# Performance work log

Hardware: AMD Instinct MI355X
Metric: run time of the kernel (lower is better)

## Reference

```python
import jax, jax.numpy as jnp
import numpy as np

B, L, H, NL, NRES = 64, 2048, 64, 10, 3
EPS = 1e-5


def _conv1d(x, w, b, pad):
    # x: [B, C, L], w: [O, I, K] (torch layout)
    y = jax.lax.conv_general_dilated(x, w, window_strides=(1,), padding=[(pad, pad)],
                                     dimension_numbers=("NCH", "OIH", "NCH"))
    return y + b[None, :, None]


def _bn(x, g, b, m, v):
    # eval-mode BatchNorm1d over channel dim of [B, C, L]
    scale = (g * jax.lax.rsqrt(v + EPS))[None, :, None]
    return (x - m[None, :, None]) * scale + b[None, :, None]


def _lstm_layer(x, w_ih, w_hh, b_ih, b_hh):
    # x: [T, B, H]; gate order (torch): i, f, g, o
    gates_x = jnp.einsum("tbh,gh->tbg", x, w_ih) + (b_ih + b_hh)  # [T, B, 4H]

    def step(carry, gx):
        h, c = carry
        gates = gx + h @ w_hh.T
        i, f, g, o = jnp.split(gates, 4, axis=-1)
        c = jax.nn.sigmoid(f) * c + jax.nn.sigmoid(i) * jnp.tanh(g)
        h = jax.nn.sigmoid(o) * jnp.tanh(c)
        return (h, c), h

    nb = x.shape[1]
    init = (jnp.zeros((nb, H), x.dtype), jnp.zeros((nb, H), x.dtype))
    _, hs = jax.lax.scan(step, init, gates_x)
    return hs  # [T, B, H]


def setup_inputs() -> dict:
    key = jax.random.key(0)
    ks = jax.random.split(key, 24)
    r = lambda i, shape, s=0.05: jax.random.normal(ks[i], shape, jnp.float32) * s
    inp = {
        "input": jax.random.normal(ks[0], (B, L, 4), jnp.float32),
        "mc": jax.random.uniform(ks[1], (B,), dtype=jnp.float32),
        "conv1_w": r(2, (32, 4, 1), 0.3), "conv1_b": r(3, (32,)),
        "conv2_w": r(4, (64, 32, 1), 0.2), "conv2_b": r(5, (64,)),
        "res_bn1_g": jnp.ones((NRES, 64), jnp.float32), "res_bn1_b": jnp.zeros((NRES, 64), jnp.float32),
        "res_bn1_m": jnp.zeros((NRES, 64), jnp.float32), "res_bn1_v": jnp.ones((NRES, 64), jnp.float32),
        "res_conv1_w": r(6, (NRES, 64, 64, 11)), "res_conv1_b": r(7, (NRES, 64)),
        "res_bn2_g": jnp.ones((NRES, 64), jnp.float32), "res_bn2_b": jnp.zeros((NRES, 64), jnp.float32),
        "res_bn2_m": jnp.zeros((NRES, 64), jnp.float32), "res_bn2_v": jnp.ones((NRES, 64), jnp.float32),
        "res_conv2_w": r(8, (NRES, 64, 64, 11)), "res_conv2_b": r(9, (NRES, 64)),
        "lstm_w_ih": r(10, (NL, 4 * H, H), 0.1), "lstm_w_hh": r(11, (NL, 4 * H, H), 0.1),
        "lstm_b_ih": r(12, (NL, 4 * H)), "lstm_b_hh": r(13, (NL, 4 * H)),
        "out_w": r(14, (H, 2), 0.1), "out_b": r(15, (2,)),
        "l": L,
    }
    return inp


def reference(input, mc, conv1_w, conv1_b, conv2_w, conv2_b,
              res_bn1_g, res_bn1_b, res_bn1_m, res_bn1_v, res_conv1_w, res_conv1_b,
              res_bn2_g, res_bn2_b, res_bn2_m, res_bn2_v, res_conv2_w, res_conv2_b,
              lstm_w_ih, lstm_w_hh, lstm_b_ih, lstm_b_hh, out_w, out_b, l):
    # mc and l are computed/accepted but never used by the original forward.
    x = jnp.transpose(input, (0, 2, 1))                    # [B, 4, L]
    x = jax.nn.relu(_conv1d(x, conv1_w, conv1_b, 0))       # [B, 32, L]
    x = jax.nn.relu(_conv1d(x, conv2_w, conv2_b, 0))       # [B, 64, L]
    for i in range(NRES):                                  # 3 pre-activation residual units
        h = jax.nn.relu(_bn(x, res_bn1_g[i], res_bn1_b[i], res_bn1_m[i], res_bn1_v[i]))
        h = _conv1d(h, res_conv1_w[i], res_conv1_b[i], 5)
        h = jax.nn.relu(_bn(h, res_bn2_g[i], res_bn2_b[i], res_bn2_m[i], res_bn2_v[i]))
        h = _conv1d(h, res_conv2_w[i], res_conv2_b[i], 5)
        x = x + h
    x = jnp.transpose(x, (2, 0, 1))                        # [L, B, 64] (seq-first, like torch LSTM)
    for layer in range(NL):
        x = _lstm_layer(x, lstm_w_ih[layer], lstm_w_hh[layer], lstm_b_ih[layer], lstm_b_hh[layer])
    logits = x[-1] @ out_w + out_b                         # [B, 2]
    return jax.nn.log_softmax(logits, axis=1)
```

## Files before the change

### kernel.cpp

```cpp
#include <hip/hip_runtime.h>
#include <hip/hip_bf16.h>

#define TL 2048
#define NB 64
#define NH 64
#define NLAY 10
#define NRESU 3
#define RSTEP 64

typedef float f32x4 __attribute__((ext_vector_type(4)));
typedef short bhalf8 __attribute__((ext_vector_type(8)));
typedef short bhalf4 __attribute__((ext_vector_type(4)));

__device__ __forceinline__ unsigned short f2bf(float f) {
    unsigned u = __float_as_uint(f);
    unsigned r = u + 0x7fffu + ((u >> 16) & 1u);
    return (unsigned short)(r >> 16);
}
__device__ __forceinline__ float bf2f(unsigned short h) {
    return __uint_as_float(((unsigned)h) << 16);
}
__device__ __forceinline__ float exp2_pos(float x) {
    float r; asm("v_exp_f32 %0, %1" : "=v"(r) : "v"(x)); return r;
}
__device__ __forceinline__ float exp2_neg(float x) {
    float r; asm("v_exp_f32 %0, -%1" : "=v"(r) : "v"(x)); return r;
}

__global__ __launch_bounds__(256) void k_frontend(
    const float* __restrict__ in,
    const float* __restrict__ c1w, const float* __restrict__ c1b,
    const float* __restrict__ c2w, const float* __restrict__ c2b,
    float* __restrict__ x0)
{
    __shared__ float s_c1w[128];
    __shared__ float s_c1b[32];
    __shared__ float s_c2w[64 * 33];
    __shared__ float s_c2b[64];
    __shared__ float h1[64 * 33];
    __shared__ float ot[64 * 65];
    int tid = threadIdx.x;
    int b = blockIdx.x >> 5;
    int l0 = (blockIdx.x & 31) << 6;
    if (tid < 128) s_c1w[tid] = c1w[tid];
    if (tid < 32) s_c1b[tid] = c1b[tid];
    if (tid < 64) s_c2b[tid] = c2b[tid];
    for (int r = tid; r < 2048; r += 256) s_c2w[(r >> 5) * 33 + (r & 31)] = c2w[r];
    __syncthreads();
    if (tid < 64) {
        const float* ip = in + ((size_t)b * TL + l0 + tid) * 4;
        float x0v = ip[0], x1 = ip[1], x2 = ip[2], x3 = ip[3];
#pragma unroll
        for (int o = 0; o < 32; o++) {
            float a = s_c1w[o * 4 + 0] * x0v + s_c1w[o * 4 + 1] * x1 +
                      s_c1w[o * 4 + 2] * x2 + s_c1w[o * 4 + 3] * x3 + s_c1b[o];
            h1[tid * 33 + o] = fmaxf(a, 0.0f);
        }
    }
    __syncthreads();
    {
        int o = tid & 63, lg = tid >> 6;
#pragma unroll
        for (int j = 0; j < 16; j++) {
            int l = lg * 16 + j;
            float a = s_c2b[o];
#pragma unroll
            for (int i = 0; i < 32; i++) a += h1[l * 33 + i] * s_c2w[o * 33 + i];
            ot[o * 65 + l] = fmaxf(a, 0.0f);
        }
    }
    __syncthreads();
    for (int r = 0; r < 16; r++) {
        int idx = tid + 256 * r;
        int c = idx >> 6, l = idx & 63;
        x0[((size_t)b * 64 + c) * TL + l0 + l] = ot[c * 65 + l];
    }
}

__global__ __launch_bounds__(256) void k_prepw_mfma(
    const float* __restrict__ w, unsigned short* __restrict__ wbh, unsigned short* __restrict__ wbl)
{
    int idx = blockIdx.x * 256 + threadIdx.x;
    if (idx >= NRESU * 11 * 64 * 64) return;
    int i = idx & 63;
    int rest = idx >> 6;
    int o = rest & 63;
    rest >>= 6;
    int k = rest % 11;
    int u = rest / 11;
    float v = w[(((size_t)u * 64 + o) * 64 + i) * 11 + k];
    unsigned short hb = f2bf(v);
    float lo = v - bf2f(hb);
    wbh[idx] = hb;
    wbl[idx] = f2bf(lo);
}

#define XTS 76
__global__ __launch_bounds__(256) void k_resconv_mfma(
    const float* __restrict__ in, float* __restrict__ out,
    const unsigned short* __restrict__ wbh, const unsigned short* __restrict__ wbl,
    const float* __restrict__ bias,
    const float* __restrict__ bg, const float* __restrict__ bb,
    const float* __restrict__ bm, const float* __restrict__ bv,
    int accumulate)
{
    __shared__ float sscale[64], sshift[64];
    __shared__ __align__(16) char smem[43776];
    unsigned short* XTH = (unsigned short*)smem;
    unsigned short* XTL = XTH + 144 * XTS;
    float* Yb = (float*)smem;

    int tid = threadIdx.x;
    int b = blockIdx.x >> 4;
    int l0 = (blockIdx.x & 15) << 7;
    int lane = tid & 63;
    int wv = tid >> 6;
    int l15 = lane & 15, l4 = lane >> 4;

    if (tid < 64) {
        float sc = bg[tid] * rsqrtf(bv[tid] + 1e-5f);
        sscale[tid] = sc;
        sshift[tid] = bb[tid] - bm[tid] * sc;
    }
    __syncthreads();

    {
        int lcol = tid & 63;
        int ib = tid >> 6;
#pragma unroll
        for (int it = 0; it < 16; it++) {
            int i = ib + it * 4;
            float sc = sscale[i], sh = sshift[i];
            const float* ip = in + ((size_t)b * 64 + i) * TL;
#pragma unroll
            for (int jc = 0; jc < 3; jc++) {
                int ll = jc * 64 + lcol;
                if (ll < 138) {
                    int l = l0 - 5 + ll;
                    float v = 0.0f;
                    if (l >= 0 && l < TL) v = fmaxf(ip[l] * sc + sh, 0.0f);
                    unsigned short hb = f2bf(v);
                    float lo = v - bf2f(hb);
                    XTH[ll * XTS + i] = hb;
                    XTL[ll * XTS + i] = f2bf(lo);
                }
            }
        }
    }
    __syncthreads();

    f32x4 acc[2][4];
#pragma unroll
    for (int s = 0; s < 2; s++)
#pragma unroll
        for (int ot = 0; ot < 4; ot++) acc[s][ot] = (f32x4){0, 0, 0, 0};

    for (int k = 0; k < 11; k++) {
#pragma unroll
        for (int ic = 0; ic < 2; ic++) {
            bhalf8 ah[2], al[2];
#pragma unroll
            for (int s = 0; s < 2; s++) {
                int row = (wv * 2 + s) * 16 + l15 + k;
                int off = row * XTS + ic * 32 + l4 * 8;
                bhalf4 h0 = *(const bhalf4*)&XTH[off];
                bhalf4 h1v = *(const bhalf4*)&XTH[off + 4];
                bhalf4 lo0 = *(const bhalf4*)&XTL[off];
                bhalf4 lo1 = *(const bhalf4*)&XTL[off + 4];
                ah[s] = (bhalf8){h0[0], h0[1], h0[2], h0[3], h1v[0], h1v[1], h1v[2], h1v[3]};
                al[s] = (bhalf8){lo0[0], lo0[1], lo0[2], lo0[3], lo1[0], lo1[1], lo1[2], lo1[3]};
            }
#pragma unroll
            for (int ot = 0; ot < 4; ot++) {
                size_t woff = ((size_t)(k * 64 + ot * 16 + l15)) * 64 + ic * 32 + l4 * 8;
                bhalf8 bh = *(const bhalf8*)&wbh[woff];
                bhalf8 bl = *(const bhalf8*)&wbl[woff];
#pragma unroll
                for (int s = 0; s < 2; s++) {
                    acc[s][ot] = __builtin_amdgcn_mfma_f32_16x16x32_bf16(ah[s], bh, acc[s][ot], 0, 0, 0);
                    acc[s][ot] = __builtin_amdgcn_mfma_f32_16x16x32_bf16(al[s], bh, acc[s][ot], 0, 0, 0);
                    acc[s][ot] = __builtin_amdgcn_mfma_f32_16x16x32_bf16(ah[s], bl, acc[s][ot], 0, 0, 0);
                }
            }
        }
    }
    __syncthreads();

#pragma unroll
    for (int s = 0; s < 2; s++)
#pragma unroll
        for (int ot = 0; ot < 4; ot++)
#pragma unroll
            for (int r = 0; r < 4; r++)
                Yb[((wv * 2 + s) * 16 + l4 * 4 + r) * 66 + ot * 16 + l15] = acc[s][ot][r];
    __syncthreads();

    {
        int o = tid >> 2, ls0 = (tid & 3) * 32;
        float bsv = bias[o];
        float* op = out + ((size_t)b * 64 + o) * TL + l0 + ls0;
        if (accumulate) {
#pragma unroll
            for (int j = 0; j < 32; j++) op[j] += Yb[(ls0 + j) * 66 + o] + bsv;
        } else {
#pragma unroll
            for (int j = 0; j < 32; j++) op[j] = Yb[(ls0 + j) * 66 + o] + bsv;
        }
    }
}

__global__ __launch_bounds__(256) void k_transpose(
    const float* __restrict__ x0, unsigned short* __restrict__ Xbf)
{
    __shared__ float t[64 * 65];
    int tid = threadIdx.x;
    int b = blockIdx.x >> 5;
    int t0 = (blockIdx.x & 31) << 6;
    for (int r = 0; r < 16; r++) {
        int idx = tid + 256 * r;
        int c = idx >> 6, tt = idx & 63;
        t[c * 65 + tt] = x0[((size_t)b * 64 + c) * TL + t0 + tt];
    }
    __syncthreads();
    for (int r = 0; r < 16; r++) {
        int idx = tid + 256 * r;
        int tt = idx >> 6, c = idx & 63;
        Xbf[((size_t)(t0 + tt)) * (NB * NH) + b * 64 + c] = f2bf(t[c * 65 + tt]);
    }
}

__global__ __launch_bounds__(512) void k_lstm(
    const unsigned short* __restrict__ Xbf,
    const float* __restrict__ w_ih, const float* __restrict__ w_hh,
    const float* __restrict__ b_ih, const float* __restrict__ b_hh,
    unsigned short* __restrict__ ring, float* __restrict__ final_h, int* prog)
{
    int bid = blockIdx.x;
    int grp = bid & 7;
    int layer = bid >> 3;
    if (grp >= 4 || layer >= NLAY) return;
    int b0 = grp * 16;
    int tid = threadIdx.x;
    int w = tid >> 6;
    int lane = tid & 63;
    int l15 = lane & 15, l4 = lane >> 4;
    int w4 = w & 3;
    int rhalf = w >> 2;
    int u = w4 * 16 + l15;
    int self = layer * 4 + grp;
    const bool has_store = (layer < NLAY - 1);
    const bool use_ring = (layer > 0);
    int brow = tid >> 5;
    int cc0 = (tid & 31) * 2;

    __shared__ __align__(16) unsigned short XH[2][16][136];

    const float LOG2E = 1.44269504f;

    bhalf8 Bh[4][4];
    float bv[4];
#pragma unroll
    for (int g = 0; g < 4; g++) {
        float wsc = (g == 2) ? 2.0f * LOG2E : LOG2E;
        int n = g * 64 + u;
        const float* rih = w_ih + ((size_t)layer * 256 + n) * 64;
        const float* rhh = w_hh + ((size_t)layer * 256 + n) * 64;
        bv[g] = (b_ih[layer * 256 + n] + b_hh[layer * 256 + n]) * wsc;
#pragma unroll
        for (int kt = 0; kt < 4; kt++) {
#pragma unroll
            for (int j = 0; j < 8; j++) {
                int k = kt * 32 + l4 * 8 + j;
                float v = (k < 64) ? rih[k] : rhh[k - 64];
                Bh[g][kt][j] = (short)f2bf(v * wsc);
            }
        }
    }
    for (int idx = tid; idx < 2 * 16 * 64; idx += 512) {
        XH[idx >> 10][(idx >> 6) & 15][64 + (idx & 63)] = 0;
    }
    float cst[2] = {0.f, 0.f};

    int* p_self = prog + self * 32;
    int* p_prev = prog + (self - 4) * 32;
    int* p_next = prog + (self + 4) * 32;
    int cached_prev = 0, cached_next = 0;

#define POLL_GE(ptr, tgt, cachev)                                                     \
    if (cachev < (tgt)) {                                                             \
        int v_; long g_ = 0;                                                          \
        while ((v_ = __hip_atomic_load(ptr, __ATOMIC_ACQUIRE,                         \
                        __HIP_MEMORY_SCOPE_AGENT)) < (tgt) && ++g_ < 1500000)         \
            __builtin_amdgcn_s_sleep(2);                                              \
        cachev = v_;                                                                  \
    }

    if (tid == 0 && layer > 0) { POLL_GE(p_prev, 32, cached_prev); }
    __syncthreads();
    unsigned px[4];
    {
        unsigned p0;
        if (!use_ring) {
            const unsigned short* s0 = Xbf + (size_t)(b0 + brow) * 64 + cc0;
            asm volatile("global_load_dword %0, %1, off" : "=&v"(p0) : "v"(s0) : "memory");
        } else {
            const unsigned short* s0 = ring + ((size_t)(layer - 1) * RSTEP) * 4096 + (b0 + brow) * 64 + cc0;
            asm volatile("global_load_dword %0, %1, off sc0 sc1" : "=&v"(p0) : "v"(s0) : "memory");
        }
        asm volatile("s_waitcnt vmcnt(0)" ::: "memory");
        __builtin_amdgcn_sched_barrier(0);
        *(unsigned*)&XH[0][brow][cc0] = p0;
#pragma unroll
        for (int pre = 1; pre <= 3; pre++) {
            if (!use_ring) {
                const unsigned short* sp = Xbf + ((size_t)pre * NB + b0 + brow) * 64 + cc0;
                asm volatile("global_load_dword %0, %1, off" : "=&v"(px[pre]) : "v"(sp) : "memory");
            } else {
                const unsigned short* sp = ring + ((size_t)(layer - 1) * RSTEP + pre) * 4096 + (b0 + brow) * 64 + cc0;
                asm volatile("global_load_dword %0, %1, off sc0 sc1" : "=&v"(px[pre]) : "v"(sp) : "memory");
            }
        }
    }
    asm volatile("s_waitcnt vmcnt(0)" ::: "memory");
    __builtin_amdgcn_sched_barrier(0);
    __syncthreads();

    for (int t0 = 0; t0 < TL; t0 += 8) {
#pragma unroll
        for (int ts = 0; ts < 8; ++ts) {
            const int p = ts & 1, q = p ^ 1;
            const int t = t0 + ts;
            const int cons = (ts + 1) & 3;
            const int pref = ts & 3;

            f32x4 acc[4];
#pragma unroll
            for (int g = 0; g < 4; g++) acc[g] = (f32x4){bv[g], bv[g], bv[g], bv[g]};
#pragma unroll
            for (int kt = 0; kt < 4; kt++) {
                bhalf8 Ah = *(const bhalf8*)&XH[p][l15][kt * 32 + l4 * 8];
                acc[0] = __builtin_amdgcn_mfma_f32_16x16x32_bf16(Ah, Bh[0][kt], acc[0], 0, 0, 0);
                acc[1] = __builtin_amdgcn_mfma_f32_16x16x32_bf16(Ah, Bh[1][kt], acc[1], 0, 0, 0);
                acc[2] = __builtin_amdgcn_mfma_f32_16x16x32_bf16(Ah, Bh[2][kt], acc[2], 0, 0, 0);
                acc[3] = __builtin_amdgcn_mfma_f32_16x16x32_bf16(Ah, Bh[3][kt], acc[3], 0, 0, 0);
            }

            float hv[2];
#pragma unroll
            for (int rr = 0; rr < 2; rr++) {
                int r = rhalf * 2 + rr;
                float si = __builtin_amdgcn_rcpf(1.0f + exp2_neg(acc[0][r]));
                float sf = __builtin_amdgcn_rcpf(1.0f + exp2_neg(acc[1][r]));
                float tg = 1.0f - 2.0f * __builtin_amdgcn_rcpf(exp2_pos(acc[2][r]) + 1.0f);
                float c = sf * cst[rr] + si * tg;
                cst[rr] = c;
                float tc = 1.0f - 2.0f * __builtin_amdgcn_rcpf(exp2_pos(c * (2.0f * LOG2E)) + 1.0f);
                float so = __builtin_amdgcn_rcpf(1.0f + exp2_neg(acc[3][r]));
                hv[rr] = so * tc;
            }
            unsigned hpk;
            asm("v_cvt_pk_bf16_f32 %0, %1, %2" : "=v"(hpk) : "v"(hv[0]), "v"(hv[1]));
            unsigned hb0 = hpk & 0xffffu;
            unsigned hb1 = hpk >> 16;

            if (has_store) { asm volatile("s_waitcnt vmcnt(6)" ::: "memory"); }
            else           { asm volatile("s_waitcnt vmcnt(2)" ::: "memory"); }
            __builtin_amdgcn_sched_barrier(0);

            *(unsigned*)&XH[q][brow][cc0] = px[cons];

            {
                int bb = l4 * 4 + rhalf * 2;
                XH[q][bb][64 + u] = (unsigned short)hb0;
                XH[q][bb + 1][64 + u] = (unsigned short)hb1;
                if (has_store) {
                    unsigned short* ap0 = ring + ((size_t)layer * RSTEP + (t & 63)) * 4096 + (b0 + bb) * 64 + u;
                    asm volatile("global_store_short %0, %1, off sc0 sc1" :: "v"(ap0), "v"(hb0) : "memory");
                    asm volatile("global_store_short %0, %1, off sc0 sc1" :: "v"(ap0 + 64), "v"(hb1) : "memory");
                } else if (t == TL - 1) {
                    final_h[(b0 + bb) * NH + u] = hv[0];
                    final_h[(b0 + bb + 1) * NH + u] = hv[1];
                }
            }

            {
                int tt = t + 4; if (tt > TL - 1) tt = TL - 1;
                if (!use_ring) {
                    const unsigned short* sp = Xbf + ((size_t)tt * NB + b0 + brow) * 64 + cc0;
                    asm volatile("global_load_dword %0, %1, off" : "=&v"(px[pref]) : "v"(sp) : "memory");
                } else {
                    const unsigned short* sp = ring + ((size_t)(layer - 1) * RSTEP + (tt & 63)) * 4096 + (b0 + brow) * 64 + cc0;
                    asm volatile("global_load_dword %0, %1, off sc0 sc1" : "=&v"(px[pref]) : "v"(sp) : "memory");
                }
            }

            asm volatile("s_waitcnt lgkmcnt(0)" ::: "memory");
            __builtin_amdgcn_s_barrier();
            __builtin_amdgcn_sched_barrier(0);
        }

        if (has_store) { asm volatile("s_waitcnt vmcnt(1)" ::: "memory"); }
        __builtin_amdgcn_s_barrier();
        __builtin_amdgcn_sched_barrier(0);
        if (tid == 0) {
            __hip_atomic_store(p_self, t0, __ATOMIC_RELEASE, __HIP_MEMORY_SCOPE_AGENT);
            int nt0 = t0 + 8;
            if (nt0 < TL) {
                if (use_ring) {
                    int tgt = nt0 + 16; if (tgt > TL) tgt = TL;
                    POLL_GE(p_prev, tgt, cached_prev);
                }
                if (has_store) {
                    int need = nt0 - 64;
                    if (need > 0) { POLL_GE(p_next, need, cached_next); }
                }
            }
        }
        __builtin_amdgcn_s_barrier();
        __builtin_amdgcn_sched_barrier(0);
    }

    asm volatile("s_waitcnt vmcnt(0)" ::: "memory");
    __builtin_amdgcn_s_barrier();
    if (tid == 0) {
        __hip_atomic_store(p_self, TL, __ATOMIC_RELEASE, __HIP_MEMORY_SCOPE_AGENT);
    }
#undef POLL_GE
}

__global__ void k_head(const float* __restrict__ fh, const float* __restrict__ ow,
                       const float* __restrict__ ob, float* __restrict__ out)
{
    int b = threadIdx.x;
    if (b >= NB) return;
    const float* h = fh + b * NH;
    float l0 = ob[0], l1 = ob[1];
    for (int uu = 0; uu < 64; uu++) { l0 += h[uu] * ow[uu * 2]; l1 += h[uu] * ow[uu * 2 + 1]; }
    float m = fmaxf(l0, l1);
    float s = expf(l0 - m) + expf(l1 - m);
    float ls = m + logf(s);
    out[b * 2] = l0 - ls;
    out[b * 2 + 1] = l1 - ls;
}

extern "C" void kernel_launch(void* const* d_in, const int* in_sizes, int n_in,
                              void* d_out, int out_size, void* d_ws, size_t ws_size,
                              hipStream_t stream) {
    const float* input = (const float*)d_in[0];
    const float* c1w = (const float*)d_in[2];
    const float* c1b = (const float*)d_in[3];
    const float* c2w = (const float*)d_in[4];
    const float* c2b = (const float*)d_in[5];
    const float* bn1g = (const float*)d_in[6];
    const float* bn1b = (const float*)d_in[7];
    const float* bn1m = (const float*)d_in[8];
    const float* bn1v = (const float*)d_in[9];
    const float* rw1 = (const float*)d_in[10];
    const float* rb1 = (const float*)d_in[11];
    const float* bn2g = (const float*)d_in[12];
    const float* bn2b = (const float*)d_in[13];
    const float* bn2m = (const float*)d_in[14];
    const float* bn2v = (const float*)d_in[15];
    const float* rw2 = (const float*)d_in[16];
    const float* rb2 = (const float*)d_in[17];
    const float* wih = (const float*)d_in[18];
    const float* whh = (const float*)d_in[19];
    const float* bih = (const float*)d_in[20];
    const float* bhh = (const float*)d_in[21];
    const float* outw = (const float*)d_in[22];
    const float* outb = (const float*)d_in[23];

    float* ws = (float*)d_ws;
    float*          x0buf = ws;
    float*          t1buf = x0buf + 8388608;
    unsigned short* Xbf   = (unsigned short*)(t1buf + 8388608);
    unsigned short* ringb = Xbf + 8388608;
    float*          fhbuf = (float*)(ringb + 2359296);
    int*            progb = (int*)(fhbuf + 4096);
    unsigned short* wbh1  = (unsigned short*)(progb + 40 * 32);
    unsigned short* wbl1  = wbh1 + NRESU * 11 * 64 * 64;
    unsigned short* wbh2  = wbl1 + NRESU * 11 * 64 * 64;
    unsigned short* wbl2  = wbh2 + NRESU * 11 * 64 * 64;

    hipMemsetAsync(progb, 0, 40 * 32 * sizeof(int), stream);

    k_prepw_mfma<<<528, 256, 0, stream>>>(rw1, wbh1, wbl1);
    k_prepw_mfma<<<528, 256, 0, stream>>>(rw2, wbh2, wbl2);
    k_frontend<<<2048, 256, 0, stream>>>(input, c1w, c1b, c2w, c2b, x0buf);
    for (int uu = 0; uu < NRESU; uu++) {
        k_resconv_mfma<<<1024, 256, 0, stream>>>(x0buf, t1buf, wbh1 + uu * 45056, wbl1 + uu * 45056,
                                                 rb1 + uu * 64, bn1g + uu * 64, bn1b + uu * 64,
                                                 bn1m + uu * 64, bn1v + uu * 64, 0);
        k_resconv_mfma<<<1024, 256, 0, stream>>>(t1buf, x0buf, wbh2 + uu * 45056, wbl2 + uu * 45056,
                                                 rb2 + uu * 64, bn2g + uu * 64, bn2b + uu * 64,
                                                 bn2m + uu * 64, bn2v + uu * 64, 1);
    }
    k_transpose<<<2048, 256, 0, stream>>>(x0buf, Xbf);
    k_lstm<<<80, 512, 0, stream>>>(Xbf, wih, whh, bih, bhh, ringb, fhbuf, progb);
    k_head<<<1, 64, 0, stream>>>(fhbuf, outw, outb, (float*)d_out);
}
```

Before: 2.672 ms.

## Split LSTM gate MFMA into input and recurrent parts, precompute next input projection

Splits the fused [x,h] x W gate matmul into an input projection (x·W_ih) and a recurrent projection (h·W_hh). The input projection for step t+1 is now computed right after step t's h is produced, so it sits off the serial recurrence path. The critical path per step drops from 16 to 8 dependent MFMAs. In exchange the x staging buffer grows to four slots, the prefetch distance goes from 4 to 6 steps, and the vmcnt wait thresholds are retuned, which adds register pressure and makes the manual wait counts more fragile.

Measured after the change: 2.675 ms. About the same (+0.1%).

```diff
diff --git a/kernel.cpp b/kernel.cpp
--- a/kernel.cpp
+++ b/kernel.cpp
@@ -253,11 +253,12 @@
     int brow = tid >> 5;
     int cc0 = (tid & 31) * 2;
 
-    __shared__ __align__(16) unsigned short XH[2][16][136];
+    __shared__ __align__(16) unsigned short XB[4][16][72];
+    __shared__ __align__(16) unsigned short HB[2][16][72];
 
     const float LOG2E = 1.44269504f;
 
-    bhalf8 Bh[4][4];
+    bhalf8 Bx[4][2], Bw[4][2];
     float bv[4];
 #pragma unroll
     for (int g = 0; g < 4; g++) {
@@ -267,17 +268,17 @@
         const float* rhh = w_hh + ((size_t)layer * 256 + n) * 64;
         bv[g] = (b_ih[layer * 256 + n] + b_hh[layer * 256 + n]) * wsc;
 #pragma unroll
-        for (int kt = 0; kt < 4; kt++) {
+        for (int kt = 0; kt < 2; kt++) {
 #pragma unroll
             for (int j = 0; j < 8; j++) {
                 int k = kt * 32 + l4 * 8 + j;
-                float v = (k < 64) ? rih[k] : rhh[k - 64];
-                Bh[g][kt][j] = (short)f2bf(v * wsc);
+                Bx[g][kt][j] = (short)f2bf(rih[k] * wsc);
+                Bw[g][kt][j] = (short)f2bf(rhh[k] * wsc);
             }
         }
     }
     for (int idx = tid; idx < 2 * 16 * 64; idx += 512) {
-        XH[idx >> 10][(idx >> 6) & 15][64 + (idx & 63)] = 0;
+        HB[idx >> 10][(idx >> 6) & 15][idx & 63] = 0;
     }
     float cst[2] = {0.f, 0.f};
 
@@ -297,28 +298,43 @@
 
     if (tid == 0 && layer > 0) { POLL_GE(p_prev, 32, cached_prev); }
     __syncthreads();
-    unsigned px[4];
     {
-        unsigned p0;
+        unsigned p0, p1;
         if (!use_ring) {
             const unsigned short* s0 = Xbf + (size_t)(b0 + brow) * 64 + cc0;
             asm volatile("global_load_dword %0, %1, off" : "=&v"(p0) : "v"(s0) : "memory");
+            asm volatile("global_load_dword %0, %1, off" : "=&v"(p1) : "v"(s0 + NB * NH) : "memory");
         } else {
             const unsigned short* s0 = ring + ((size_t)(layer - 1) * RSTEP) * 4096 + (b0 + brow) * 64 + cc0;
             asm volatile("global_load_dword %0, %1, off sc0 sc1" : "=&v"(p0) : "v"(s0) : "memory");
+            asm volatile("global_load_dword %0, %1, off sc0 sc1" : "=&v"(p1) : "v"(s0 + 4096) : "memory");
         }
         asm volatile("s_waitcnt vmcnt(0)" ::: "memory");
         __builtin_amdgcn_sched_barrier(0);
-        *(unsigned*)&XH[0][brow][cc0] = p0;
-#pragma unroll
-        for (int pre = 1; pre <= 3; pre++) {
-            if (!use_ring) {
-                const unsigned short* sp = Xbf + ((size_t)pre * NB + b0 + brow) * 64 + cc0;
-                asm volatile("global_load_dword %0, %1, off" : "=&v"(px[pre]) : "v"(sp) : "memory");
-            } else {
-                const unsigned short* sp = ring + ((size_t)(layer - 1) * RSTEP + pre) * 4096 + (b0 + brow) * 64 + cc0;
-                asm volatile("global_load_dword %0, %1, off sc0 sc1" : "=&v"(px[pre]) : "v"(sp) : "memory");
-            }
+        *(unsigned*)&XB[0][brow][cc0] = p0;
+        *(unsigned*)&XB[1][brow][cc0] = p1;
+    }
+    __syncthreads();
+    f32x4 xac[4];
+#pragma unroll
+    for (int g = 0; g < 4; g++) xac[g] = (f32x4){bv[g], bv[g], bv[g], bv[g]};
+#pragma unroll
+    for (int kt = 0; kt < 2; kt++) {
+        bhalf8 Ax = *(const bhalf8*)&XB[0][l15][kt * 32 + l4 * 8];
+        xac[0] = __builtin_amdgcn_mfma_f32_16x16x32_bf16(Ax, Bx[0][kt], xac[0], 0, 0, 0);
+        xac[1] = __builtin_amdgcn_mfma_f32_16x16x32_bf16(Ax, Bx[1][kt], xac[1], 0, 0, 0);
+        xac[2] = __builtin_amdgcn_mfma_f32_16x16x32_bf16(Ax, Bx[2][kt], xac[2], 0, 0, 0);
+        xac[3] = __builtin_amdgcn_mfma_f32_16x16x32_bf16(Ax, Bx[3][kt], xac[3], 0, 0, 0);
+    }
+    unsigned px[4];
+#pragma unroll
+    for (int pre = 2; pre <= 5; pre++) {
+        if (!use_ring) {
+            const unsigned short* sp = Xbf + ((size_t)pre * NB + b0 + brow) * 64 + cc0;
+            asm volatile("global_load_dword %0, %1, off" : "=&v"(px[pre & 3]) : "v"(sp) : "memory");
+        } else {
+            const unsigned short* sp = ring + ((size_t)(layer - 1) * RSTEP + pre) * 4096 + (b0 + brow) * 64 + cc0;
+            asm volatile("global_load_dword %0, %1, off sc0 sc1" : "=&v"(px[pre & 3]) : "v"(sp) : "memory");
         }
     }
     asm volatile("s_waitcnt vmcnt(0)" ::: "memory");
@@ -330,32 +346,30 @@
         for (int ts = 0; ts < 8; ++ts) {
             const int p = ts & 1, q = p ^ 1;
             const int t = t0 + ts;
-            const int cons = (ts + 1) & 3;
-            const int pref = ts & 3;
-
-            f32x4 acc[4];
-#pragma unroll
-            for (int g = 0; g < 4; g++) acc[g] = (f32x4){bv[g], bv[g], bv[g], bv[g]};
-#pragma unroll
-            for (int kt = 0; kt < 4; kt++) {
-                bhalf8 Ah = *(const bhalf8*)&XH[p][l15][kt * 32 + l4 * 8];
-                acc[0] = __builtin_amdgcn_mfma_f32_16x16x32_bf16(Ah, Bh[0][kt], acc[0], 0, 0, 0);
-                acc[1] = __builtin_amdgcn_mfma_f32_16x16x32_bf16(Ah, Bh[1][kt], acc[1], 0, 0, 0);
-                acc[2] = __builtin_amdgcn_mfma_f32_16x16x32_bf16(Ah, Bh[2][kt], acc[2], 0, 0, 0);
-                acc[3] = __builtin_amdgcn_mfma_f32_16x16x32_bf16(Ah, Bh[3][kt], acc[3], 0, 0, 0);
+            const int xs = (ts + 2) & 3;
+            const int xn = (ts + 1) & 3;
+
+            f32x4 hac0 = xac[0], hac1 = xac[1], hac2 = xac[2], hac3 = xac[3];
+#pragma unroll
+            for (int kt = 0; kt < 2; kt++) {
+                bhalf8 Ah = *(const bhalf8*)&HB[p][l15][kt * 32 + l4 * 8];
+                hac0 = __builtin_amdgcn_mfma_f32_16x16x32_bf16(Ah, Bw[0][kt], hac0, 0, 0, 0);
+                hac1 = __builtin_amdgcn_mfma_f32_16x16x32_bf16(Ah, Bw[1][kt], hac1, 0, 0, 0);
+                hac2 = __builtin_amdgcn_mfma_f32_16x16x32_bf16(Ah, Bw[2][kt], hac2, 0, 0, 0);
+                hac3 = __builtin_amdgcn_mfma_f32_16x16x32_bf16(Ah, Bw[3][kt], hac3, 0, 0, 0);
             }
 
             float hv[2];
 #pragma unroll
             for (int rr = 0; rr < 2; rr++) {
                 int r = rhalf * 2 + rr;
-                float si = __builtin_amdgcn_rcpf(1.0f + exp2_neg(acc[0][r]));
-                float sf = __builtin_amdgcn_rcpf(1.0f + exp2_neg(acc[1][r]));
-                float tg = 1.0f - 2.0f * __builtin_amdgcn_rcpf(exp2_pos(acc[2][r]) + 1.0f);
+                float si = __builtin_amdgcn_rcpf(1.0f + exp2_neg(hac0[r]));
+                float sf = __builtin_amdgcn_rcpf(1.0f + exp2_neg(hac1[r]));
+                float tg = 1.0f - 2.0f * __builtin_amdgcn_rcpf(exp2_pos(hac2[r]) + 1.0f);
                 float c = sf * cst[rr] + si * tg;
                 cst[rr] = c;
                 float tc = 1.0f - 2.0f * __builtin_amdgcn_rcpf(exp2_pos(c * (2.0f * LOG2E)) + 1.0f);
-                float so = __builtin_amdgcn_rcpf(1.0f + exp2_neg(acc[3][r]));
+                float so = __builtin_amdgcn_rcpf(1.0f + exp2_neg(hac3[r]));
                 hv[rr] = so * tc;
             }
             unsigned hpk;
@@ -363,16 +377,16 @@
             unsigned hb0 = hpk & 0xffffu;
             unsigned hb1 = hpk >> 16;
 
-            if (has_store) { asm volatile("s_waitcnt vmcnt(6)" ::: "memory"); }
-            else           { asm volatile("s_waitcnt vmcnt(2)" ::: "memory"); }
+            if (has_store) { asm volatile("s_waitcnt vmcnt(9)" ::: "memory"); }
+            else           { asm volatile("s_waitcnt vmcnt(3)" ::: "memory"); }
             __builtin_amdgcn_sched_barrier(0);
 
-            *(unsigned*)&XH[q][brow][cc0] = px[cons];
+            *(unsigned*)&XB[xs][brow][cc0] = px[xs];
 
             {
                 int bb = l4 * 4 + rhalf * 2;
-                XH[q][bb][64 + u] = (unsigned short)hb0;
-                XH[q][bb + 1][64 + u] = (unsigned short)hb1;
+                HB[q][bb][u] = (unsigned short)hb0;
+                HB[q][bb + 1][u] = (unsigned short)hb1;
                 if (has_store) {
                     unsigned short* ap0 = ring + ((size_t)layer * RSTEP + (t & 63)) * 4096 + (b0 + bb) * 64 + u;
                     asm volatile("global_store_short %0, %1, off sc0 sc1" :: "v"(ap0), "v"(hb0) : "memory");
@@ -384,14 +398,25 @@
             }
 
             {
-                int tt = t + 4; if (tt > TL - 1) tt = TL - 1;
+                int tt = t + 6; if (tt > TL - 1) tt = TL - 1;
                 if (!use_ring) {
                     const unsigned short* sp = Xbf + ((size_t)tt * NB + b0 + brow) * 64 + cc0;
-                    asm volatile("global_load_dword %0, %1, off" : "=&v"(px[pref]) : "v"(sp) : "memory");
+                    asm volatile("global_load_dword %0, %1, off" : "=&v"(px[xs]) : "v"(sp) : "memory");
                 } else {
                     const unsigned short* sp = ring + ((size_t)(layer - 1) * RSTEP + (tt & 63)) * 4096 + (b0 + brow) * 64 + cc0;
-                    asm volatile("global_load_dword %0, %1, off sc0 sc1" : "=&v"(px[pref]) : "v"(sp) : "memory");
+                    asm volatile("global_load_dword %0, %1, off sc0 sc1" : "=&v"(px[xs]) : "v"(sp) : "memory");
                 }
+            }
+
+#pragma unroll
+            for (int g = 0; g < 4; g++) xac[g] = (f32x4){bv[g], bv[g], bv[g], bv[g]};
+#pragma unroll
+            for (int kt = 0; kt < 2; kt++) {
+                bhalf8 Ax = *(const bhalf8*)&XB[xn][l15][kt * 32 + l4 * 8];
+                xac[0] = __builtin_amdgcn_mfma_f32_16x16x32_bf16(Ax, Bx[0][kt], xac[0], 0, 0, 0);
+                xac[1] = __builtin_amdgcn_mfma_f32_16x16x32_bf16(Ax, Bx[1][kt], xac[1], 0, 0, 0);
+                xac[2] = __builtin_amdgcn_mfma_f32_16x16x32_bf16(Ax, Bx[2][kt], xac[2], 0, 0, 0);
+                xac[3] = __builtin_amdgcn_mfma_f32_16x16x32_bf16(Ax, Bx[3][kt], xac[3], 0, 0, 0);
             }
 
             asm volatile("s_waitcnt lgkmcnt(0)" ::: "memory");
```

## Merge two LSTM batch groups into one 1024-thread block per layer

Applied to the files above, without the earlier changes.

Each LSTM block now holds two 16-batch groups (1024 threads) instead of one, so each layer runs on 2 blocks instead of 4, with a separate shared-memory slice per group. The block-wide s_barrier now spans both groups, so the two independent recurrences are coupled per timestep and the slower one sets the pace. This halves the number of active CUs and doubles the waves sharing one CU's MFMA and transcendental units, in exchange for fewer blocks. Progress flags are still written per group by each half's leader thread.

After: 4.038 ms. 51.1% more time.

```diff
diff --git a/kernel.cpp b/kernel.cpp
--- a/kernel.cpp
+++ b/kernel.cpp
@@ -229,19 +229,22 @@
     }
 }
 
-__global__ __launch_bounds__(512) void k_lstm(
+__global__ __launch_bounds__(1024) void k_lstm(
     const unsigned short* __restrict__ Xbf,
     const float* __restrict__ w_ih, const float* __restrict__ w_hh,
     const float* __restrict__ b_ih, const float* __restrict__ b_hh,
     unsigned short* __restrict__ ring, float* __restrict__ final_h, int* prog)
 {
     int bid = blockIdx.x;
-    int grp = bid & 7;
+    int pair = bid & 7;
     int layer = bid >> 3;
-    if (grp >= 4 || layer >= NLAY) return;
+    if (pair >= 2 || layer >= NLAY) return;
+    int tid = threadIdx.x;
+    int g2 = tid >> 9;
+    int tg = tid & 511;
+    int grp = pair * 2 + g2;
     int b0 = grp * 16;
-    int tid = threadIdx.x;
-    int w = tid >> 6;
+    int w = tg >> 6;
     int lane = tid & 63;
     int l15 = lane & 15, l4 = lane >> 4;
     int w4 = w & 3;
@@ -250,10 +253,10 @@
     int self = layer * 4 + grp;
     const bool has_store = (layer < NLAY - 1);
     const bool use_ring = (layer > 0);
-    int brow = tid >> 5;
-    int cc0 = (tid & 31) * 2;
-
-    __shared__ __align__(16) unsigned short XH[2][16][136];
+    int brow = tg >> 5;
+    int cc0 = (tg & 31) * 2;
+
+    __shared__ __align__(16) unsigned short XH[2][2][16][136];
 
     const float LOG2E = 1.44269504f;
 
@@ -276,8 +279,11 @@
             }
         }
     }
-    for (int idx = tid; idx < 2 * 16 * 64; idx += 512) {
-        XH[idx >> 10][(idx >> 6) & 15][64 + (idx & 63)] = 0;
+    for (int idx = tid; idx < 2 * 2 * 16 * 64; idx += 1024) {
+        int gg = idx >> 11;
+        int bufb = (idx >> 10) & 1;
+        int rw = (idx >> 6) & 15;
+        XH[gg][bufb][rw][64 + (idx & 63)] = 0;
     }
     float cst[2] = {0.f, 0.f};
 
@@ -295,7 +301,7 @@
         cachev = v_;                                                                  \
     }
 
-    if (tid == 0 && layer > 0) { POLL_GE(p_prev, 32, cached_prev); }
+    if (tg == 0 && layer > 0) { POLL_GE(p_prev, 32, cached_prev); }
     __syncthreads();
     unsigned px[4];
     {
@@ -309,7 +315,7 @@
         }
         asm volatile("s_waitcnt vmcnt(0)" ::: "memory");
         __builtin_amdgcn_sched_barrier(0);
-        *(unsigned*)&XH[0][brow][cc0] = p0;
+        *(unsigned*)&XH[g2][0][brow][cc0] = p0;
 #pragma unroll
         for (int pre = 1; pre <= 3; pre++) {
             if (!use_ring) {
@@ -338,7 +344,7 @@
             for (int g = 0; g < 4; g++) acc[g] = (f32x4){bv[g], bv[g], bv[g], bv[g]};
 #pragma unroll
             for (int kt = 0; kt < 4; kt++) {
-                bhalf8 Ah = *(const bhalf8*)&XH[p][l15][kt * 32 + l4 * 8];
+                bhalf8 Ah = *(const bhalf8*)&XH[g2][p][l15][kt * 32 + l4 * 8];
                 acc[0] = __builtin_amdgcn_mfma_f32_16x16x32_bf16(Ah, Bh[0][kt], acc[0], 0, 0, 0);
                 acc[1] = __builtin_amdgcn_mfma_f32_16x16x32_bf16(Ah, Bh[1][kt], acc[1], 0, 0, 0);
                 acc[2] = __builtin_amdgcn_mfma_f32_16x16x32_bf16(Ah, Bh[2][kt], acc[2], 0, 0, 0);
@@ -351,8 +357,8 @@
                 int r = rhalf * 2 + rr;
                 float si = __builtin_amdgcn_rcpf(1.0f + exp2_neg(acc[0][r]));
                 float sf = __builtin_amdgcn_rcpf(1.0f + exp2_neg(acc[1][r]));
-                float tg = 1.0f - 2.0f * __builtin_amdgcn_rcpf(exp2_pos(acc[2][r]) + 1.0f);
-                float c = sf * cst[rr] + si * tg;
+                float tg2 = 1.0f - 2.0f * __builtin_amdgcn_rcpf(exp2_pos(acc[2][r]) + 1.0f);
+                float c = sf * cst[rr] + si * tg2;
                 cst[rr] = c;
                 float tc = 1.0f - 2.0f * __builtin_amdgcn_rcpf(exp2_pos(c * (2.0f * LOG2E)) + 1.0f);
                 float so = __builtin_amdgcn_rcpf(1.0f + exp2_neg(acc[3][r]));
@@ -367,12 +373,12 @@
             else           { asm volatile("s_waitcnt vmcnt(2)" ::: "memory"); }
             __builtin_amdgcn_sched_barrier(0);
 
-            *(unsigned*)&XH[q][brow][cc0] = px[cons];
+            *(unsigned*)&XH[g2][q][brow][cc0] = px[cons];
 
             {
                 int bb = l4 * 4 + rhalf * 2;
-                XH[q][bb][64 + u] = (unsigned short)hb0;
-                XH[q][bb + 1][64 + u] = (unsigned short)hb1;
+                XH[g2][q][bb][64 + u] = (unsigned short)hb0;
+                XH[g2][q][bb + 1][64 + u] = (unsigned short)hb1;
                 if (has_store) {
                     unsigned short* ap0 = ring + ((size_t)layer * RSTEP + (t & 63)) * 4096 + (b0 + bb) * 64 + u;
                     asm volatile("global_store_short %0, %1, off sc0 sc1" :: "v"(ap0), "v"(hb0) : "memory");
@@ -402,7 +408,7 @@
         if (has_store) { asm volatile("s_waitcnt vmcnt(1)" ::: "memory"); }
         __builtin_amdgcn_s_barrier();
         __builtin_amdgcn_sched_barrier(0);
-        if (tid == 0) {
+        if (tg == 0) {
             __hip_atomic_store(p_self, t0, __ATOMIC_RELEASE, __HIP_MEMORY_SCOPE_AGENT);
             int nt0 = t0 + 8;
             if (nt0 < TL) {
@@ -422,7 +428,7 @@
 
     asm volatile("s_waitcnt vmcnt(0)" ::: "memory");
     __builtin_amdgcn_s_barrier();
-    if (tid == 0) {
+    if (tg == 0) {
         __hip_atomic_store(p_self, TL, __ATOMIC_RELEASE, __HIP_MEMORY_SCOPE_AGENT);
     }
 #undef POLL_GE
@@ -496,6 +502,6 @@
                                                  bn2m + uu * 64, bn2v + uu * 64, 1);
     }
     k_transpose<<<2048, 256, 0, stream>>>(x0buf, Xbf);
-    k_lstm<<<80, 512, 0, stream>>>(Xbf, wih, whh, bih, bhh, ringb, fhbuf, progb);
+    k_lstm<<<80, 1024, 0, stream>>>(Xbf, wih, whh, bih, bhh, ringb, fhbuf, progb);
     k_head<<<1, 64, 0, stream>>>(fhbuf, outw, outb, (float*)d_out);
 }
```
